# Performance work log

Measured on AMD Instinct MI355X. Metric: run time of the kernel, lower is better.

## Reference

```python
import jax, jax.numpy as jnp
import numpy as np

N_NODES = 50000
N_EDGES = 800000
IN_NODE = 64
IN_EDGE = 32
HIDDEN = 128
NUM_LAYERS = 3
OUT_DIM = 8
NUM_GRAPHS = 128


def setup_inputs() -> dict:
    key = jax.random.key(0)
    ks = jax.random.split(key, 20)
    inp = {
        "x": jax.random.normal(ks[0], (N_NODES, IN_NODE), dtype=jnp.float32),
        "edge_index": jax.random.randint(ks[1], (2, N_EDGES), 0, N_NODES, dtype=jnp.int32),
        "edge_attr": jax.random.normal(ks[2], (N_EDGES, IN_EDGE), dtype=jnp.float32),
        "batch": jnp.sort(jax.random.randint(ks[3], (N_NODES,), 0, NUM_GRAPHS, dtype=jnp.int32)),
    }
    # MLP params per GINEConv layer: Linear(d_in, H) -> ReLU -> Linear(H, H)
    d_ins = [IN_NODE + IN_EDGE] + [HIDDEN + IN_EDGE] * (NUM_LAYERS - 1)
    for i, d_in in enumerate(d_ins):
        inp[f"w{i}_1"] = jax.random.normal(ks[4 + 3 * i], (d_in, HIDDEN), dtype=jnp.float32) * (1.0 / np.sqrt(d_in))
        inp[f"b{i}_1"] = jnp.zeros((HIDDEN,), dtype=jnp.float32)
        inp[f"w{i}_2"] = jax.random.normal(ks[5 + 3 * i], (HIDDEN, HIDDEN), dtype=jnp.float32) * (1.0 / np.sqrt(HIDDEN))
        inp[f"b{i}_2"] = jnp.zeros((HIDDEN,), dtype=jnp.float32)
    inp["lin_w"] = jax.random.normal(ks[15], (HIDDEN, OUT_DIM), dtype=jnp.float32) * (1.0 / np.sqrt(HIDDEN))
    inp["lin_b"] = jnp.zeros((OUT_DIM,), dtype=jnp.float32)
    return inp


def _gine_conv(x, src, dst, edge_attr, w1, b1, w2, b2):
    # gather source node feats, concat with edge feats, 2-layer MLP, scatter-add to dst
    m = jnp.concatenate([x[src], edge_attr], axis=-1)        # [E, d_in]
    h = jax.nn.relu(m @ w1 + b1) @ w2 + b2                   # [E, H]
    return jax.ops.segment_sum(h, dst, num_segments=N_NODES)  # [N, H]


def reference(x, edge_index, edge_attr, batch,
              w0_1, b0_1, w0_2, b0_2,
              w1_1, b1_1, w1_2, b1_2,
              w2_1, b2_1, w2_2, b2_2,
              lin_w, lin_b):
    src, dst = edge_index[0], edge_index[1]
    layers = [(w0_1, b0_1, w0_2, b0_2), (w1_1, b1_1, w1_2, b1_2), (w2_1, b2_1, w2_2, b2_2)]
    h = x
    for (w1, b1, w2, b2) in layers:
        h = jax.nn.relu(_gine_conv(h, src, dst, edge_attr, w1, b1, w2, b2))
    # global mean pool over graphs
    sums = jax.ops.segment_sum(h, batch, num_segments=NUM_GRAPHS)          # [G, H]
    cnts = jax.ops.segment_sum(jnp.ones((N_NODES,), h.dtype), batch, num_segments=NUM_GRAPHS)
    pooled = sums / jnp.maximum(cnts, 1.0)[:, None]
    return pooled @ lin_w + lin_b
```

## Files before the change

kernel.cpp:

```cpp
#include <hip/hip_runtime.h>
#include <hip/hip_bf16.h>
#include <stdint.h>

typedef __attribute__((ext_vector_type(8))) __bf16 bf16x8;
typedef __attribute__((ext_vector_type(4))) __bf16 bf16x4;
typedef __attribute__((ext_vector_type(4))) float f32x4;

static constexpr int NN = 50000;
static constexpr int NE = 800000;
static constexpr int FX = 64;
static constexpr int FE = 32;
static constexpr int H  = 128;
static constexpr int NG = 128;
static constexpr int OD = 8;

__global__ void cvt_f32_bf16(const float* __restrict__ in, __bf16* __restrict__ out, int n) {
  int idx = (blockIdx.x * blockDim.x + threadIdx.x) * 4;
  if (idx + 3 < n) {
    float4 v = *reinterpret_cast<const float4*>(in + idx);
    bf16x4 o;
    o[0] = (__bf16)v.x; o[1] = (__bf16)v.y; o[2] = (__bf16)v.z; o[3] = (__bf16)v.w;
    *reinterpret_cast<bf16x4*>(out + idx) = o;
  } else {
    for (; idx < n; ++idx) out[idx] = (__bf16)in[idx];
  }
}

__global__ void cvt_w_all(const float* __restrict__ a0, const float* __restrict__ a1,
                          const float* __restrict__ a2, const float* __restrict__ a3,
                          const float* __restrict__ a4, const float* __restrict__ a5,
                          __bf16* __restrict__ o0, __bf16* __restrict__ o1,
                          __bf16* __restrict__ o2, __bf16* __restrict__ o3,
                          __bf16* __restrict__ o4, __bf16* __restrict__ o5) {
  int i = blockIdx.x * blockDim.x + threadIdx.x;
  const float* src; __bf16* dst; int K; int base;
  if      (i <  12288) { src = a0; dst = o0; K =  96; base = 0; }
  else if (i <  32768) { src = a1; dst = o1; K = 160; base = 12288; }
  else if (i <  53248) { src = a2; dst = o2; K = 160; base = 32768; }
  else if (i <  69632) { src = a3; dst = o3; K = 128; base = 53248; }
  else if (i <  86016) { src = a4; dst = o4; K = 128; base = 69632; }
  else if (i < 102400) { src = a5; dst = o5; K = 128; base = 86016; }
  else return;
  int j = i - base;
  int n = j / K, k = j % K;
  dst[j] = (__bf16)src[k * 128 + n];
}

__global__ void hist_build(const int* __restrict__ dst, int* __restrict__ hist) {
  int e = blockIdx.x * blockDim.x + threadIdx.x;
  if (e < NE) atomicAdd(&hist[dst[e]], 1);
}

__global__ void scan1(const int* __restrict__ hist, int* __restrict__ excl, int* __restrict__ btot) {
  __shared__ int tmp[256];
  int t = threadIdx.x;
  int i = blockIdx.x * 256 + t;
  int v = (i < NN) ? hist[i] : 0;
  tmp[t] = v;
  __syncthreads();
  for (int off = 1; off < 256; off <<= 1) {
    int add = (t >= off) ? tmp[t - off] : 0;
    __syncthreads();
    tmp[t] += add;
    __syncthreads();
  }
  if (i < NN) excl[i] = tmp[t] - v;
  if (t == 255) btot[blockIdx.x] = tmp[255];
}

__global__ void scan2(int* __restrict__ btot, int nb) {
  __shared__ int tmp[256];
  int t = threadIdx.x;
  int v = (t < nb) ? btot[t] : 0;
  tmp[t] = v;
  __syncthreads();
  for (int off = 1; off < 256; off <<= 1) {
    int add = (t >= off) ? tmp[t - off] : 0;
    __syncthreads();
    tmp[t] += add;
    __syncthreads();
  }
  if (t < nb) btot[t] = tmp[t] - v;
}

__global__ void scan3(const int* __restrict__ excl, const int* __restrict__ btot,
                      int* __restrict__ cursor) {
  int i = blockIdx.x * 256 + threadIdx.x;
  if (i < NN) cursor[i] = excl[i] + btot[blockIdx.x];
}

__global__ void scatter_perm_ea(const int* __restrict__ src, const int* __restrict__ dst,
                                const float* __restrict__ ea,
                                int* __restrict__ cursor,
                                int* __restrict__ srcp, int* __restrict__ dstp,
                                __bf16* __restrict__ eabs) {
  int e = blockIdx.x * blockDim.x + threadIdx.x;
  if (e >= NE) return;
  int d = dst[e];
  int p = atomicAdd(&cursor[d], 1);
  srcp[p] = src[e];
  dstp[p] = d;
  const float* er = ea + (size_t)e * FE;
  __bf16* op = eabs + (size_t)p * FE;
#pragma unroll
  for (int c = 0; c < 4; ++c) {
    float4 v0 = *reinterpret_cast<const float4*>(er + c * 8);
    float4 v1 = *reinterpret_cast<const float4*>(er + c * 8 + 4);
    bf16x8 o;
    o[0] = (__bf16)v0.x; o[1] = (__bf16)v0.y; o[2] = (__bf16)v0.z; o[3] = (__bf16)v0.w;
    o[4] = (__bf16)v1.x; o[5] = (__bf16)v1.y; o[6] = (__bf16)v1.z; o[7] = (__bf16)v1.w;
    *reinterpret_cast<bf16x8*>(op + c * 8) = o;
  }
}

template<int F, int DIN>
__global__ __launch_bounds__(512) void node_gemm2(
    const __bf16* __restrict__ Ain,
    const __bf16* __restrict__ wt,
    __bf16* __restrict__ Y)
{
  constexpr int APAD = F + 8;
  constexpr int KS   = F / 32;
  constexpr int CH   = F / 8;
  constexpr int AB   = 128 * APAD * 2;
  constexpr int OB   = 128 * 136 * 2;
  constexpr int SB   = (AB > OB) ? AB : OB;
  __shared__ __align__(16) char smem[SB];
  auto As  = reinterpret_cast<__bf16 (*)[APAD]>(smem);
  auto Ost = reinterpret_cast<__bf16 (*)[136]>(smem);

  const int tid   = threadIdx.x;
  const int lane  = tid & 63;
  const int w     = tid >> 6;
  const int m0    = blockIdx.x * 128;
  const int colq  = lane & 15;
  const int krow  = (lane >> 4) * 8;
  const int rbase = (lane >> 4) * 4;
  const int col   = w * 16 + colq;

  bf16x8 bf[KS];
#pragma unroll
  for (int ks = 0; ks < KS; ++ks)
    bf[ks] = *reinterpret_cast<const bf16x8*>(wt + (size_t)col * DIN + ks * 32 + krow);

  for (int i = tid; i < 128 * CH; i += 512) {
    int row = i / CH, c = i % CH;
    int g = m0 + row; if (g >= NN) g = NN - 1;
    *reinterpret_cast<bf16x8*>(&As[row][c * 8]) =
        *reinterpret_cast<const bf16x8*>(Ain + (size_t)g * F + c * 8);
  }
  __syncthreads();

  f32x4 acc[8];
#pragma unroll
  for (int mt = 0; mt < 8; ++mt) acc[mt] = (f32x4){0.f, 0.f, 0.f, 0.f};
#pragma unroll
  for (int ks = 0; ks < KS; ++ks)
#pragma unroll
    for (int mt = 0; mt < 8; ++mt) {
      bf16x8 a = *reinterpret_cast<const bf16x8*>(&As[mt * 16 + colq][ks * 32 + krow]);
      acc[mt] = __builtin_amdgcn_mfma_f32_16x16x32_bf16(a, bf[ks], acc[mt], 0, 0, 0);
    }
  __syncthreads();

#pragma unroll
  for (int mt = 0; mt < 8; ++mt)
#pragma unroll
    for (int r = 0; r < 4; ++r)
      Ost[mt * 16 + rbase + r][col] = (__bf16)acc[mt][r];
  __syncthreads();

  for (int i = tid; i < 128 * 16; i += 512) {
    int row = i >> 4, c = i & 15;
    int g = m0 + row;
    if (g < NN)
      *reinterpret_cast<bf16x8*>(Y + (size_t)g * H + c * 8) =
          *reinterpret_cast<const bf16x8*>(&Ost[row][c * 8]);
  }
}

__global__ __launch_bounds__(512) void node_wy_t(
    float* __restrict__ aggH,
    const int* __restrict__ deg,
    const __bf16* __restrict__ w2t,
    const float* __restrict__ b2,
    const __bf16* __restrict__ w1t,
    __bf16* __restrict__ Y)
{
  __shared__ __bf16 Ast[128][136];
  __shared__ __bf16 Hst[128][136];
  __shared__ int deg_s[128];

  const int tid   = threadIdx.x;
  const int lane  = tid & 63;
  const int w     = tid >> 6;
  const int m0    = blockIdx.x * 128;
  const int colq  = lane & 15;
  const int krow  = (lane >> 4) * 8;
  const int rbase = (lane >> 4) * 4;
  const int col   = w * 16 + colq;

  for (int i = tid; i < 128 * 16; i += 512) {
    int row = i >> 4, cb = (i & 15) * 8;
    int g = m0 + row;
    bool valid = g < NN;
    int gc = valid ? g : NN - 1;
    float* s = aggH + (size_t)gc * H + cb;
    float4 v0 = *reinterpret_cast<const float4*>(s);
    float4 v1 = *reinterpret_cast<const float4*>(s + 4);
    bf16x8 o;
    o[0] = (__bf16)v0.x; o[1] = (__bf16)v0.y; o[2] = (__bf16)v0.z; o[3] = (__bf16)v0.w;
    o[4] = (__bf16)v1.x; o[5] = (__bf16)v1.y; o[6] = (__bf16)v1.z; o[7] = (__bf16)v1.w;
    *reinterpret_cast<bf16x8*>(&Ast[row][cb]) = o;
    if (valid) {
      *reinterpret_cast<float4*>(s)     = (float4){0.f, 0.f, 0.f, 0.f};
      *reinterpret_cast<float4*>(s + 4) = (float4){0.f, 0.f, 0.f, 0.f};
    }
  }
  if (tid < 128) {
    int g = m0 + tid;
    deg_s[tid] = (g < NN) ? deg[g] : 0;
  }
  __syncthreads();

  bf16x8 w2f[4];
#pragma unroll
  for (int ks = 0; ks < 4; ++ks)
    w2f[ks] = *reinterpret_cast<const bf16x8*>(w2t + (size_t)col * H + ks * 32 + krow);
  const float b2s = b2[col];

  f32x4 acc[8];
#pragma unroll
  for (int mt = 0; mt < 8; ++mt) acc[mt] = (f32x4){0.f, 0.f, 0.f, 0.f};
#pragma unroll
  for (int ks = 0; ks < 4; ++ks)
#pragma unroll
    for (int mt = 0; mt < 8; ++mt) {
      bf16x8 a = *reinterpret_cast<const bf16x8*>(&Ast[mt * 16 + colq][ks * 32 + krow]);
      acc[mt] = __builtin_amdgcn_mfma_f32_16x16x32_bf16(a, w2f[ks], acc[mt], 0, 0, 0);
    }

#pragma unroll
  for (int mt = 0; mt < 8; ++mt)
#pragma unroll
    for (int r = 0; r < 4; ++r) {
      int row = mt * 16 + rbase + r;
      float v = acc[mt][r] + (float)deg_s[row] * b2s;
      Hst[row][col] = (__bf16)fmaxf(v, 0.f);
    }
  __syncthreads();

  bf16x8 w1f[4];
#pragma unroll
  for (int ks = 0; ks < 4; ++ks)
    w1f[ks] = *reinterpret_cast<const bf16x8*>(w1t + (size_t)col * 160 + ks * 32 + krow);

  f32x4 acc2[8];
#pragma unroll
  for (int mt = 0; mt < 8; ++mt) acc2[mt] = (f32x4){0.f, 0.f, 0.f, 0.f};
#pragma unroll
  for (int ks = 0; ks < 4; ++ks)
#pragma unroll
    for (int mt = 0; mt < 8; ++mt) {
      bf16x8 a = *reinterpret_cast<const bf16x8*>(&Hst[mt * 16 + colq][ks * 32 + krow]);
      acc2[mt] = __builtin_amdgcn_mfma_f32_16x16x32_bf16(a, w1f[ks], acc2[mt], 0, 0, 0);
    }

#pragma unroll
  for (int mt = 0; mt < 8; ++mt)
#pragma unroll
    for (int r = 0; r < 4; ++r)
      Ast[mt * 16 + rbase + r][col] = (__bf16)acc2[mt][r];
  __syncthreads();

  for (int i = tid; i < 128 * 16; i += 512) {
    int row = i >> 4, cb = (i & 15) * 8;
    int g = m0 + row;
    if (g < NN)
      *reinterpret_cast<bf16x8*>(Y + (size_t)g * H + cb) =
          *reinterpret_cast<const bf16x8*>(&Ast[row][cb]);
  }
}

__global__ __launch_bounds__(512) void node_pool(
    const float* __restrict__ aggH,
    const int* __restrict__ deg,
    const __bf16* __restrict__ w2t,
    const float* __restrict__ b2,
    const int* __restrict__ batch,
    float* __restrict__ sums)
{
  __shared__ __bf16 Ast[128][136];
  __shared__ int deg_s[128];
  __shared__ int bs[128];

  const int tid   = threadIdx.x;
  const int lane  = tid & 63;
  const int w     = tid >> 6;
  const int m0    = blockIdx.x * 128;
  const int colq  = lane & 15;
  const int krow  = (lane >> 4) * 8;
  const int rbase = (lane >> 4) * 4;
  const int col   = w * 16 + colq;

  for (int i = tid; i < 128 * 16; i += 512) {
    int row = i >> 4, cb = (i & 15) * 8;
    int g = m0 + row; if (g >= NN) g = NN - 1;
    const float* s = aggH + (size_t)g * H + cb;
    float4 v0 = *reinterpret_cast<const float4*>(s);
    float4 v1 = *reinterpret_cast<const float4*>(s + 4);
    bf16x8 o;
    o[0] = (__bf16)v0.x; o[1] = (__bf16)v0.y; o[2] = (__bf16)v0.z; o[3] = (__bf16)v0.w;
    o[4] = (__bf16)v1.x; o[5] = (__bf16)v1.y; o[6] = (__bf16)v1.z; o[7] = (__bf16)v1.w;
    *reinterpret_cast<bf16x8*>(&Ast[row][cb]) = o;
  }
  if (tid < 128) {
    int g = m0 + tid;
    deg_s[tid] = (g < NN) ? deg[g] : 0;
    bs[tid]    = (g < NN) ? batch[g] : -1;
  }
  __syncthreads();

  bf16x8 w2f[4];
#pragma unroll
  for (int ks = 0; ks < 4; ++ks)
    w2f[ks] = *reinterpret_cast<const bf16x8*>(w2t + (size_t)col * H + ks * 32 + krow);
  const float b2s = b2[col];

  f32x4 acc[8];
#pragma unroll
  for (int mt = 0; mt < 8; ++mt) acc[mt] = (f32x4){0.f, 0.f, 0.f, 0.f};
#pragma unroll
  for (int ks = 0; ks < 4; ++ks)
#pragma unroll
    for (int mt = 0; mt < 8; ++mt) {
      bf16x8 a = *reinterpret_cast<const bf16x8*>(&Ast[mt * 16 + colq][ks * 32 + krow]);
      acc[mt] = __builtin_amdgcn_mfma_f32_16x16x32_bf16(a, w2f[ks], acc[mt], 0, 0, 0);
    }

  float run = 0.f;
  int cur = -2;
#pragma unroll
  for (int mt = 0; mt < 8; ++mt)
#pragma unroll
    for (int r = 0; r < 4; ++r) {
      int row = mt * 16 + rbase + r;
      int b = bs[row];
      float v = fmaxf(acc[mt][r] + (float)deg_s[row] * b2s, 0.f);
      if (b != cur) {
        if (cur >= 0) atomicAdd(&sums[cur * H + col], run);
        run = 0.f;
        cur = b;
      }
      if (b >= 0) run += v;
    }
  if (cur >= 0) atomicAdd(&sums[cur * H + col], run);
}

template<int DIN>
__global__ __launch_bounds__(512) void edge_mlp4(
    const __bf16* __restrict__ Yb,
    const __bf16* __restrict__ eabs,
    const int* __restrict__ srcp, const int* __restrict__ dstp,
    const __bf16* __restrict__ w1t,
    const float* __restrict__ b1,
    float* __restrict__ aggH,
    int ntiles)
{
  constexpr int F = DIN - 32;
  constexpr int TPB = 4;
  __shared__ __bf16 Ylds[128][128];
  __shared__ int dst_s[128];

  const int tid   = threadIdx.x;
  const int lane  = tid & 63;
  const int w     = tid >> 6;
  const int colq  = lane & 15;
  const int krow  = (lane >> 4) * 8;
  const int rbase = (lane >> 4) * 4;
  const int col   = w * 16 + colq;

  const bf16x8 b1f = *reinterpret_cast<const bf16x8*>(w1t + (size_t)col * DIN + F + krow);
  const float  b1s = b1[col];

  const int yrow = tid >> 4;
  const int yc   = tid & 15;
  const int drow = tid & 127;

  int t0 = blockIdx.x * TPB;
  int t1 = t0 + TPB; if (t1 > ntiles) t1 = ntiles;
  if (t0 >= ntiles) return;

  int e0 = t0 * 128;
  int sA[4];
#pragma unroll
  for (int k = 0; k < 4; ++k) sA[k] = srcp[e0 + yrow + 32 * k];
  int dreg = dstp[e0 + drow];
  bf16x8 yreg[4];
#pragma unroll
  for (int k = 0; k < 4; ++k)
    yreg[k] = *reinterpret_cast<const bf16x8*>(Yb + (size_t)sA[k] * H + yc * 8);
  bf16x8 aef[8];
#pragma unroll
  for (int mt = 0; mt < 8; ++mt)
    aef[mt] = *reinterpret_cast<const bf16x8*>(eabs + (size_t)(e0 + mt * 16 + colq) * FE + krow);
  {
    int e0n = (t0 + 1 < t1) ? (t0 + 1) * 128 : e0;
#pragma unroll
    for (int k = 0; k < 4; ++k) sA[k] = srcp[e0n + yrow + 32 * k];
  }

  for (int t = t0; t < t1; ++t) {
    __syncthreads();
#pragma unroll
    for (int k = 0; k < 4; ++k) {
      int row = yrow + 32 * k;
      int cb = (yc * 8 + ((row >> 2) & 3) * 16) & 127;
      *reinterpret_cast<bf16x8*>(&Ylds[row][cb]) = yreg[k];
    }
    if (tid < 128) dst_s[tid] = dreg;
    __syncthreads();

    if (t + 1 < t1) {
      int e1 = (t + 1) * 128;
#pragma unroll
      for (int k = 0; k < 4; ++k)
        yreg[k] = *reinterpret_cast<const bf16x8*>(Yb + (size_t)sA[k] * H + yc * 8);
      dreg = dstp[e1 + drow];
      int e2 = (t + 2 < t1) ? (t + 2) * 128 : e1;
#pragma unroll
      for (int k = 0; k < 4; ++k) sA[k] = srcp[e2 + yrow + 32 * k];
    }

    f32x4 acc[8];
#pragma unroll
    for (int mt = 0; mt < 8; ++mt) acc[mt] = (f32x4){b1s, b1s, b1s, b1s};
#pragma unroll
    for (int mt = 0; mt < 8; ++mt)
      acc[mt] = __builtin_amdgcn_mfma_f32_16x16x32_bf16(aef[mt], b1f, acc[mt], 0, 0, 0);

    if (t + 1 < t1) {
      int e1 = (t + 1) * 128;
#pragma unroll
      for (int mt = 0; mt < 8; ++mt)
        aef[mt] = *reinterpret_cast<const bf16x8*>(eabs + (size_t)(e1 + mt * 16 + colq) * FE + krow);
    }

#pragma unroll
    for (int mt = 0; mt < 8; ++mt)
#pragma unroll
      for (int r = 0; r < 4; ++r) {
        int row = mt * 16 + rbase + r;
        int cs = (col + ((row >> 2) & 3) * 16) & 127;
        float v = (float)Ylds[row][cs] + acc[mt][r];
        Ylds[row][cs] = (__bf16)fmaxf(v, 0.f);
      }
    __syncthreads();

    {
      const int rc = tid & 127;
      const int r0 = (tid >> 7) * 32;
      float s = 0.f;
      int d = dst_s[r0];
#pragma unroll 4
      for (int r = r0; r < r0 + 32; ++r) {
        int dn = dst_s[r];
        float v = (float)Ylds[r][(rc + ((r >> 2) & 3) * 16) & 127];
        if (dn != d) { atomicAdd(aggH + (size_t)d * H + rc, s); s = 0.f; d = dn; }
        s += v;
      }
      atomicAdd(aggH + (size_t)d * H + rc, s);
    }
  }
}

__global__ void final_kernel(const float* __restrict__ sums, const int* __restrict__ batch,
                             const float* __restrict__ lw, const float* __restrict__ lb,
                             float* __restrict__ out) {
  int idx = blockIdx.x * blockDim.x + threadIdx.x;
  if (idx >= NG * OD) return;
  int g = idx / OD, o = idx % OD;
  auto lbs = [&](int key) {
    int lo = 0, hi = NN;
    while (lo < hi) {
      int mid = (lo + hi) >> 1;
      if (batch[mid] < key) lo = mid + 1; else hi = mid;
    }
    return lo;
  };
  int c = lbs(g + 1) - lbs(g);
  float inv = 1.f / fmaxf((float)c, 1.f);
  float s = 0.f;
#pragma unroll 8
  for (int k = 0; k < H; ++k)
    s += sums[g * H + k] * lw[k * OD + o];
  out[idx] = s * inv + lb[o];
}

extern "C" void kernel_launch(void* const* d_in, const int* in_sizes, int n_in,
                              void* d_out, int out_size, void* d_ws, size_t ws_size,
                              hipStream_t stream) {
  const float* x   = (const float*)d_in[0];
  const int*   ei  = (const int*)d_in[1];
  const float* ea  = (const float*)d_in[2];
  const int*   bat = (const int*)d_in[3];
  const float* w1[3] = {(const float*)d_in[4], (const float*)d_in[8],  (const float*)d_in[12]};
  const float* b1[3] = {(const float*)d_in[5], (const float*)d_in[9],  (const float*)d_in[13]};
  const float* w2[3] = {(const float*)d_in[6], (const float*)d_in[10], (const float*)d_in[14]};
  const float* b2[3] = {(const float*)d_in[7], (const float*)d_in[11], (const float*)d_in[15]};
  const float* lw  = (const float*)d_in[16];
  const float* lb  = (const float*)d_in[17];
  float* out = (float*)d_out;

  char* ws = (char*)d_ws;
  size_t off = 0;
  auto alloc = [&](size_t bytes) -> void* {
    void* p = ws + off;
    off = (off + bytes + 255) & ~(size_t)255;
    return p;
  };
  __bf16* xb   = (__bf16*)alloc((size_t)NN * FX * 2);
  __bf16* Yb   = (__bf16*)alloc((size_t)NN * H * 2);
  __bf16* eabs = (__bf16*)alloc((size_t)NE * FE * 2);
  float*  agg  = (float*) alloc((size_t)NN * H * 4);
  __bf16* w1t[3]; __bf16* w2t[3];
  for (int l = 0; l < 3; ++l) {
    w1t[l] = (__bf16*)alloc(128 * 160 * 2);
    w2t[l] = (__bf16*)alloc(128 * 128 * 2);
  }
  float* sums = (float*)alloc(NG * H * 4);
  int* hist   = (int*)alloc((size_t)NN * 4);
  int* excl   = (int*)alloc((size_t)NN * 4);
  int* btot   = (int*)alloc(256 * 4);
  int* cursor = (int*)alloc((size_t)NN * 4);
  int* srcp   = (int*)alloc((size_t)NE * 4);
  int* dstp   = (int*)alloc((size_t)NE * 4);

  const int* src = ei;
  const int* dst = ei + NE;
  const int NB_SCAN = (NN + 255) / 256;
  const int NTILES = NE / 128;
  const int EGRID  = (NTILES + 3) / 4;
  const int NGRID  = (NN + 127) / 128;

  hipMemsetAsync(agg, 0, (size_t)NN * H * 4, stream);
  hipMemsetAsync(sums, 0, (size_t)NG * H * 4, stream);

  cvt_f32_bf16<<<(NN * FX / 4 + 255) / 256, 256, 0, stream>>>(x, xb, NN * FX);
  cvt_w_all<<<(102400 + 255) / 256, 256, 0, stream>>>(
      w1[0], w1[1], w1[2], w2[0], w2[1], w2[2],
      w1t[0], w1t[1], w1t[2], w2t[0], w2t[1], w2t[2]);

  hipMemsetAsync(hist, 0, (size_t)NN * 4, stream);
  hist_build<<<(NE + 255) / 256, 256, 0, stream>>>(dst, hist);
  scan1<<<NB_SCAN, 256, 0, stream>>>(hist, excl, btot);
  scan2<<<1, 256, 0, stream>>>(btot, NB_SCAN);
  scan3<<<NB_SCAN, 256, 0, stream>>>(excl, btot, cursor);
  scatter_perm_ea<<<(NE + 255) / 256, 256, 0, stream>>>(src, dst, ea, cursor, srcp, dstp, eabs);

  node_gemm2<64, 96><<<NGRID, 512, 0, stream>>>(xb, w1t[0], Yb);
  edge_mlp4<96><<<EGRID, 512, 0, stream>>>(Yb, eabs, srcp, dstp, w1t[0], b1[0], agg, NTILES);

  for (int l = 1; l < 3; ++l) {
    node_wy_t<<<NGRID, 512, 0, stream>>>(agg, hist, w2t[l - 1], b2[l - 1], w1t[l], Yb);
    edge_mlp4<160><<<EGRID, 512, 0, stream>>>(Yb, eabs, srcp, dstp, w1t[l], b1[l], agg, NTILES);
  }

  node_pool<<<NGRID, 512, 0, stream>>>(agg, hist, w2t[2], b2[2], bat, sums);
  final_kernel<<<(NG * OD + 255) / 256, 256, 0, stream>>>(sums, bat, lw, lb, out);
}
```

Baseline: 422.1 us.

## Gather Y directly into MFMA register layout, drop LDS staging in edge kernel

The edge MLP kernel no longer stages gathered source-node rows and destination indices through shared memory. Each lane instead loads the bf16 Y values it needs as scalar 2-byte gathers that match the MFMA accumulator layout, then does the ReLU and the segmented atomic scatter straight from registers. This removes three barriers per tile and the LDS round trips. In exchange, the coalesced 16-byte row loads become many scattered 2-byte loads, the Y and edge-attribute prefetch for the next tile is dropped, and more atomics are issued because each lane's run spans only 4 rows per 16-row group.

```diff
diff --git a/kernel.cpp b/kernel.cpp
--- a/kernel.cpp
+++ b/kernel.cpp
@@ -358,7 +358,7 @@
 }
 
 template<int DIN>
-__global__ __launch_bounds__(512) void edge_mlp4(
+__global__ __launch_bounds__(512) void edge_mlp6(
     const __bf16* __restrict__ Yb,
     const __bf16* __restrict__ eabs,
     const int* __restrict__ srcp, const int* __restrict__ dstp,
@@ -369,67 +369,51 @@
 {
   constexpr int F = DIN - 32;
   constexpr int TPB = 4;
-  __shared__ __bf16 Ylds[128][128];
-  __shared__ int dst_s[128];
-
-  const int tid   = threadIdx.x;
-  const int lane  = tid & 63;
-  const int w     = tid >> 6;
-  const int colq  = lane & 15;
-  const int krow  = (lane >> 4) * 8;
-  const int rbase = (lane >> 4) * 4;
-  const int col   = w * 16 + colq;
+  const int tid  = threadIdx.x;
+  const int lane = tid & 63;
+  const int w    = tid >> 6;
+  const int colq = lane & 15;
+  const int q    = lane >> 4;
+  const int krow = q * 8;
+  const int col  = w * 16 + colq;
 
   const bf16x8 b1f = *reinterpret_cast<const bf16x8*>(w1t + (size_t)col * DIN + F + krow);
   const float  b1s = b1[col];
-
-  const int yrow = tid >> 4;
-  const int yc   = tid & 15;
-  const int drow = tid & 127;
 
   int t0 = blockIdx.x * TPB;
   int t1 = t0 + TPB; if (t1 > ntiles) t1 = ntiles;
   if (t0 >= ntiles) return;
 
-  int e0 = t0 * 128;
-  int sA[4];
-#pragma unroll
-  for (int k = 0; k < 4; ++k) sA[k] = srcp[e0 + yrow + 32 * k];
-  int dreg = dstp[e0 + drow];
-  bf16x8 yreg[4];
-#pragma unroll
-  for (int k = 0; k < 4; ++k)
-    yreg[k] = *reinterpret_cast<const bf16x8*>(Yb + (size_t)sA[k] * H + yc * 8);
-  bf16x8 aef[8];
+  int4 s4[8];
 #pragma unroll
   for (int mt = 0; mt < 8; ++mt)
-    aef[mt] = *reinterpret_cast<const bf16x8*>(eabs + (size_t)(e0 + mt * 16 + colq) * FE + krow);
-  {
-    int e0n = (t0 + 1 < t1) ? (t0 + 1) * 128 : e0;
-#pragma unroll
-    for (int k = 0; k < 4; ++k) sA[k] = srcp[e0n + yrow + 32 * k];
-  }
+    s4[mt] = *reinterpret_cast<const int4*>(srcp + t0 * 128 + mt * 16 + q * 4);
 
   for (int t = t0; t < t1; ++t) {
-    __syncthreads();
-#pragma unroll
-    for (int k = 0; k < 4; ++k) {
-      int row = yrow + 32 * k;
-      int cb = (yc * 8 + ((row >> 2) & 3) * 16) & 127;
-      *reinterpret_cast<bf16x8*>(&Ylds[row][cb]) = yreg[k];
-    }
-    if (tid < 128) dst_s[tid] = dreg;
-    __syncthreads();
+    const int e0 = t * 128;
+
+    unsigned short yv[8][4];
+#pragma unroll
+    for (int mt = 0; mt < 8; ++mt) {
+#pragma unroll
+      for (int r = 0; r < 4; ++r) {
+        int sv = reinterpret_cast<const int*>(&s4[mt])[r];
+        yv[mt][r] = *(reinterpret_cast<const unsigned short*>(Yb) + (size_t)sv * H + col);
+      }
+    }
+
+    bf16x8 aef[8];
+    int4 d4[8];
+#pragma unroll
+    for (int mt = 0; mt < 8; ++mt) {
+      aef[mt] = *reinterpret_cast<const bf16x8*>(eabs + (size_t)(e0 + mt * 16 + colq) * FE + krow);
+      d4[mt]  = *reinterpret_cast<const int4*>(dstp + e0 + mt * 16 + q * 4);
+    }
 
     if (t + 1 < t1) {
-      int e1 = (t + 1) * 128;
-#pragma unroll
-      for (int k = 0; k < 4; ++k)
-        yreg[k] = *reinterpret_cast<const bf16x8*>(Yb + (size_t)sA[k] * H + yc * 8);
-      dreg = dstp[e1 + drow];
-      int e2 = (t + 2 < t1) ? (t + 2) * 128 : e1;
-#pragma unroll
-      for (int k = 0; k < 4; ++k) sA[k] = srcp[e2 + yrow + 32 * k];
+#pragma unroll
+      for (int mt = 0; mt < 8; ++mt)
+        s4[mt] = *reinterpret_cast<const int4*>(srcp + (e0 + 128) + mt * 16 + q * 4);
     }
 
     f32x4 acc[8];
@@ -439,38 +423,24 @@
     for (int mt = 0; mt < 8; ++mt)
       acc[mt] = __builtin_amdgcn_mfma_f32_16x16x32_bf16(aef[mt], b1f, acc[mt], 0, 0, 0);
 
-    if (t + 1 < t1) {
-      int e1 = (t + 1) * 128;
-#pragma unroll
-      for (int mt = 0; mt < 8; ++mt)
-        aef[mt] = *reinterpret_cast<const bf16x8*>(eabs + (size_t)(e1 + mt * 16 + colq) * FE + krow);
-    }
-
-#pragma unroll
-    for (int mt = 0; mt < 8; ++mt)
+    float run = 0.f;
+    int cur = reinterpret_cast<const int*>(&d4[0])[0];
+#pragma unroll
+    for (int mt = 0; mt < 8; ++mt) {
 #pragma unroll
       for (int r = 0; r < 4; ++r) {
-        int row = mt * 16 + rbase + r;
-        int cs = (col + ((row >> 2) & 3) * 16) & 127;
-        float v = (float)Ylds[row][cs] + acc[mt][r];
-        Ylds[row][cs] = (__bf16)fmaxf(v, 0.f);
+        int d  = reinterpret_cast<const int*>(&d4[mt])[r];
+        float yf = __uint_as_float(((unsigned)yv[mt][r]) << 16);
+        float v  = fmaxf(yf + acc[mt][r], 0.f);
+        if (d != cur) {
+          atomicAdd(aggH + (size_t)cur * H + col, run);
+          run = 0.f;
+          cur = d;
+        }
+        run += v;
       }
-    __syncthreads();
-
-    {
-      const int rc = tid & 127;
-      const int r0 = (tid >> 7) * 32;
-      float s = 0.f;
-      int d = dst_s[r0];
-#pragma unroll 4
-      for (int r = r0; r < r0 + 32; ++r) {
-        int dn = dst_s[r];
-        float v = (float)Ylds[r][(rc + ((r >> 2) & 3) * 16) & 127];
-        if (dn != d) { atomicAdd(aggH + (size_t)d * H + rc, s); s = 0.f; d = dn; }
-        s += v;
-      }
-      atomicAdd(aggH + (size_t)d * H + rc, s);
-    }
+    }
+    atomicAdd(aggH + (size_t)cur * H + col, run);
   }
 }
 
@@ -559,11 +529,11 @@
   scatter_perm_ea<<<(NE + 255) / 256, 256, 0, stream>>>(src, dst, ea, cursor, srcp, dstp, eabs);
 
   node_gemm2<64, 96><<<NGRID, 512, 0, stream>>>(xb, w1t[0], Yb);
-  edge_mlp4<96><<<EGRID, 512, 0, stream>>>(Yb, eabs, srcp, dstp, w1t[0], b1[0], agg, NTILES);
+  edge_mlp6<96><<<EGRID, 512, 0, stream>>>(Yb, eabs, srcp, dstp, w1t[0], b1[0], agg, NTILES);
 
   for (int l = 1; l < 3; ++l) {
     node_wy_t<<<NGRID, 512, 0, stream>>>(agg, hist, w2t[l - 1], b2[l - 1], w1t[l], Yb);
-    edge_mlp4<160><<<EGRID, 512, 0, stream>>>(Yb, eabs, srcp, dstp, w1t[l], b1[l], agg, NTILES);
+    edge_mlp6<160><<<EGRID, 512, 0, stream>>>(Yb, eabs, srcp, dstp, w1t[l], b1[l], agg, NTILES);
   }
 
   node_pool<<<NGRID, 512, 0, stream>>>(agg, hist, w2t[2], b2[2], bat, sums);
```

Result: slower. 939.1 us (+122.5%).

## Retile edge MLP kernel to 64-edge tiles with 256-thread blocks

Applied to the files above, without the earlier changes.

The edge MLP kernel now processes 64-edge tiles with 256 threads. Each wave covers 32 output columns through two MFMA column tiles instead of one, and each block walks 8 tiles instead of 4. This halves LDS use per block and should let more blocks and waves reside per CU, improving latency hiding for the gathered Y rows and the atomic scatter. The cost is shorter segment runs per tile, which may mean more atomics, and more per-tile sync overhead relative to the work done.

```diff
diff --git a/kernel.cpp b/kernel.cpp
--- a/kernel.cpp
+++ b/kernel.cpp
@@ -358,7 +358,7 @@
 }
 
 template<int DIN>
-__global__ __launch_bounds__(512) void edge_mlp4(
+__global__ __launch_bounds__(256) void edge_mlp7(
     const __bf16* __restrict__ Yb,
     const __bf16* __restrict__ eabs,
     const int* __restrict__ srcp, const int* __restrict__ dstp,
@@ -368,93 +368,108 @@
     int ntiles)
 {
   constexpr int F = DIN - 32;
-  constexpr int TPB = 4;
-  __shared__ __bf16 Ylds[128][128];
-  __shared__ int dst_s[128];
+  constexpr int TPB = 8;
+  __shared__ __bf16 Ylds[64][128];
+  __shared__ int dst_s[64];
 
   const int tid   = threadIdx.x;
   const int lane  = tid & 63;
   const int w     = tid >> 6;
   const int colq  = lane & 15;
-  const int krow  = (lane >> 4) * 8;
-  const int rbase = (lane >> 4) * 4;
-  const int col   = w * 16 + colq;
-
-  const bf16x8 b1f = *reinterpret_cast<const bf16x8*>(w1t + (size_t)col * DIN + F + krow);
-  const float  b1s = b1[col];
+  const int q     = lane >> 4;
+  const int krow  = q * 8;
+  const int rbase = q * 4;
+
+  bf16x8 b1f[2];
+  float  b1s[2];
+  int    cols[2];
+#pragma unroll
+  for (int nt = 0; nt < 2; ++nt) {
+    cols[nt] = w * 32 + nt * 16 + colq;
+    b1f[nt] = *reinterpret_cast<const bf16x8*>(w1t + (size_t)cols[nt] * DIN + F + krow);
+    b1s[nt] = b1[cols[nt]];
+  }
 
   const int yrow = tid >> 4;
   const int yc   = tid & 15;
-  const int drow = tid & 127;
+  const int drow = tid & 63;
 
   int t0 = blockIdx.x * TPB;
   int t1 = t0 + TPB; if (t1 > ntiles) t1 = ntiles;
   if (t0 >= ntiles) return;
 
-  int e0 = t0 * 128;
+  int e0 = t0 * 64;
   int sA[4];
 #pragma unroll
-  for (int k = 0; k < 4; ++k) sA[k] = srcp[e0 + yrow + 32 * k];
+  for (int k = 0; k < 4; ++k) sA[k] = srcp[e0 + yrow + 16 * k];
   int dreg = dstp[e0 + drow];
   bf16x8 yreg[4];
 #pragma unroll
   for (int k = 0; k < 4; ++k)
     yreg[k] = *reinterpret_cast<const bf16x8*>(Yb + (size_t)sA[k] * H + yc * 8);
-  bf16x8 aef[8];
-#pragma unroll
-  for (int mt = 0; mt < 8; ++mt)
+  bf16x8 aef[4];
+#pragma unroll
+  for (int mt = 0; mt < 4; ++mt)
     aef[mt] = *reinterpret_cast<const bf16x8*>(eabs + (size_t)(e0 + mt * 16 + colq) * FE + krow);
   {
-    int e0n = (t0 + 1 < t1) ? (t0 + 1) * 128 : e0;
-#pragma unroll
-    for (int k = 0; k < 4; ++k) sA[k] = srcp[e0n + yrow + 32 * k];
+    int e0n = (t0 + 1 < t1) ? (t0 + 1) * 64 : e0;
+#pragma unroll
+    for (int k = 0; k < 4; ++k) sA[k] = srcp[e0n + yrow + 16 * k];
   }
 
   for (int t = t0; t < t1; ++t) {
     __syncthreads();
 #pragma unroll
     for (int k = 0; k < 4; ++k) {
-      int row = yrow + 32 * k;
+      int row = yrow + 16 * k;
       int cb = (yc * 8 + ((row >> 2) & 3) * 16) & 127;
       *reinterpret_cast<bf16x8*>(&Ylds[row][cb]) = yreg[k];
     }
-    if (tid < 128) dst_s[tid] = dreg;
+    if (tid < 64) dst_s[tid] = dreg;
     __syncthreads();
 
     if (t + 1 < t1) {
-      int e1 = (t + 1) * 128;
+      int e1 = (t + 1) * 64;
 #pragma unroll
       for (int k = 0; k < 4; ++k)
         yreg[k] = *reinterpret_cast<const bf16x8*>(Yb + (size_t)sA[k] * H + yc * 8);
       dreg = dstp[e1 + drow];
-      int e2 = (t + 2 < t1) ? (t + 2) * 128 : e1;
-#pragma unroll
-      for (int k = 0; k < 4; ++k) sA[k] = srcp[e2 + yrow + 32 * k];
-    }
-
-    f32x4 acc[8];
-#pragma unroll
-    for (int mt = 0; mt < 8; ++mt) acc[mt] = (f32x4){b1s, b1s, b1s, b1s};
-#pragma unroll
-    for (int mt = 0; mt < 8; ++mt)
-      acc[mt] = __builtin_amdgcn_mfma_f32_16x16x32_bf16(aef[mt], b1f, acc[mt], 0, 0, 0);
+      int e2 = (t + 2 < t1) ? (t + 2) * 64 : e1;
+#pragma unroll
+      for (int k = 0; k < 4; ++k) sA[k] = srcp[e2 + yrow + 16 * k];
+    }
+
+    f32x4 acc[4][2];
+#pragma unroll
+    for (int mt = 0; mt < 4; ++mt)
+#pragma unroll
+      for (int nt = 0; nt < 2; ++nt)
+        acc[mt][nt] = (f32x4){b1s[nt], b1s[nt], b1s[nt], b1s[nt]};
+#pragma unroll
+    for (int mt = 0; mt < 4; ++mt) {
+      acc[mt][0] = __builtin_amdgcn_mfma_f32_16x16x32_bf16(aef[mt], b1f[0], acc[mt][0], 0, 0, 0);
+      acc[mt][1] = __builtin_amdgcn_mfma_f32_16x16x32_bf16(aef[mt], b1f[1], acc[mt][1], 0, 0, 0);
+    }
 
     if (t + 1 < t1) {
-      int e1 = (t + 1) * 128;
-#pragma unroll
-      for (int mt = 0; mt < 8; ++mt)
+      int e1 = (t + 1) * 64;
+#pragma unroll
+      for (int mt = 0; mt < 4; ++mt)
         aef[mt] = *reinterpret_cast<const bf16x8*>(eabs + (size_t)(e1 + mt * 16 + colq) * FE + krow);
     }
 
 #pragma unroll
-    for (int mt = 0; mt < 8; ++mt)
-#pragma unroll
-      for (int r = 0; r < 4; ++r) {
-        int row = mt * 16 + rbase + r;
-        int cs = (col + ((row >> 2) & 3) * 16) & 127;
-        float v = (float)Ylds[row][cs] + acc[mt][r];
-        Ylds[row][cs] = (__bf16)fmaxf(v, 0.f);
-      }
+    for (int nt = 0; nt < 2; ++nt) {
+      const int cs = (cols[nt] + q * 16) & 127;
+#pragma unroll
+      for (int mt = 0; mt < 4; ++mt)
+#pragma unroll
+        for (int r = 0; r < 4; ++r) {
+          int row = mt * 16 + rbase + r;
+          float v = (float)Ylds[row][cs] + acc[mt][nt][r];
+          Ylds[row][cs] = (__bf16)fmaxf(v, 0.f);
+        }
+    }
     __syncthreads();
 
     {
@@ -539,8 +554,8 @@
   const int* src = ei;
   const int* dst = ei + NE;
   const int NB_SCAN = (NN + 255) / 256;
-  const int NTILES = NE / 128;
-  const int EGRID  = (NTILES + 3) / 4;
+  const int NTILES = NE / 64;
+  const int EGRID  = (NTILES + 7) / 8;
   const int NGRID  = (NN + 127) / 128;
 
   hipMemsetAsync(agg, 0, (size_t)NN * H * 4, stream);
@@ -559,11 +574,11 @@
   scatter_perm_ea<<<(NE + 255) / 256, 256, 0, stream>>>(src, dst, ea, cursor, srcp, dstp, eabs);
 
   node_gemm2<64, 96><<<NGRID, 512, 0, stream>>>(xb, w1t[0], Yb);
-  edge_mlp4<96><<<EGRID, 512, 0, stream>>>(Yb, eabs, srcp, dstp, w1t[0], b1[0], agg, NTILES);
+  edge_mlp7<96><<<EGRID, 256, 0, stream>>>(Yb, eabs, srcp, dstp, w1t[0], b1[0], agg, NTILES);
 
   for (int l = 1; l < 3; ++l) {
     node_wy_t<<<NGRID, 512, 0, stream>>>(agg, hist, w2t[l - 1], b2[l - 1], w1t[l], Yb);
-    edge_mlp4<160><<<EGRID, 512, 0, stream>>>(Yb, eabs, srcp, dstp, w1t[l], b1[l], agg, NTILES);
+    edge_mlp7<160><<<EGRID, 256, 0, stream>>>(Yb, eabs, srcp, dstp, w1t[l], b1[l], agg, NTILES);
   }
 
   node_pool<<<NGRID, 512, 0, stream>>>(agg, hist, w2t[2], b2[2], bat, sums);
```

Measured after the change: 434.7 us. +3.0%, slower.
